# Optimization experiments

Measured on AMD Instinct MI355X. Metric: run time of the kernel, lower is better.

The kernel has to match this reference:

```python
import jax, jax.numpy as jnp
import numpy as np


def setup_inputs() -> dict:
    key = jax.random.key(0)
    kq, kk, kv = jax.random.split(key, 3)
    B, T, H, D = 2, 4096, 8, 64
    q = jax.random.normal(kq, (B, T, H, D), dtype=jnp.float32)
    k = jax.random.normal(kk, (B, T, H, D), dtype=jnp.float32)
    v = jax.random.normal(kv, (B, T, H, D), dtype=jnp.float32)
    return {"q": q, "k": k, "v": v}


def reference(q, k, v):
    """Linear matrix-memory recurrence over the sequence:
       M_t = M_{t-1} + v_t k_t^T ;  y_t = M_t q_t
    q, k, v: [B, T, H, D] -> y: [B, T, H, D]
    """
    B, T, H, D = q.shape
    # time-major for scan: [T, B, H, D]
    qT = jnp.moveaxis(q, 1, 0)
    kT = jnp.moveaxis(k, 1, 0)
    vT = jnp.moveaxis(v, 1, 0)

    def step(M, qkv):
        q_t, k_t, v_t = qkv  # each [B, H, D]
        # update: M += v_t k_t^T  (outer product, 'bhd,bhe->bhde')
        M = M + v_t[..., :, None] * k_t[..., None, :]
        # apply: y_t = M q_t  ('bhde,bhe->bhd')
        y_t = jnp.einsum('bhde,bhe->bhd', M, q_t)
        return M, y_t

    M0 = jnp.zeros((B, H, D, D), dtype=q.dtype)
    _, ys = jax.lax.scan(step, M0, (qT, kT, vT))  # ys: [T, B, H, D]
    return jnp.moveaxis(ys, 0, 1)  # [B, T, H, D]
```

## Files before the change

kernel.cpp:

```cpp
#include <hip/hip_runtime.h>


#define B_   2
#define T_   4096
#define H_   8
#define D_   64
#define CH   64
#define NC   (T_ / CH)
#define BH   (B_ * H_)
#define SROW (H_ * D_)
#define SB   (T_ * H_ * D_)

typedef __attribute__((ext_vector_type(4))) float f32x4;
typedef __attribute__((ext_vector_type(8))) short bf16x8;

__device__ inline unsigned short f2bf(float f) {
  unsigned int u = __builtin_bit_cast(unsigned int, f);
  unsigned int r = (u + 0x7FFFu + ((u >> 16) & 1u)) >> 16;
  return (unsigned short)r;
}
__device__ inline float bf2f(unsigned short b) {
  unsigned int u = ((unsigned int)b) << 16;
  return __builtin_bit_cast(float, u);
}
__device__ inline void st4bf(unsigned short* p, float a, float b, float c, float d) {
  union { uint2 u; unsigned short s[4]; } x;
  x.s[0] = f2bf(a); x.s[1] = f2bf(b); x.s[2] = f2bf(c); x.s[3] = f2bf(d);
  *(uint2*)p = x.u;
}
__device__ inline bf16x8 ld128(const unsigned short* p) {
  union { uint4 u; bf16x8 v; } x;
  x.u = *(const uint4*)p;
  return x.v;
}


__global__ __launch_bounds__(256) void k_chunksum(const float* __restrict__ kp,
                                                  const float* __restrict__ vp,
                                                  float* __restrict__ W) {
  const int bid = blockIdx.x;
  const int c   = bid % NC;
  const int bh  = bid / NC;
  const int b   = bh / H_, h = bh % H_;
  const size_t base = (size_t)b * SB + (size_t)h * D_ + (size_t)(c * CH) * SROW;

  __shared__ __align__(16) unsigned short KH[4096], KL[4096], VH[4096], VL[4096];

  const int tid = threadIdx.x;
  const int l = tid & 63, w = tid >> 6;
  const int mlan = l & 15, qlan = l >> 4;

  {
    const int t0 = (tid >> 4) * 4;
    const int m0 = tid & 15;
    const int qs = (t0 >> 3) & 3, kbs = t0 >> 5, j0 = t0 & 4;
    float4 kr[4], vr[4];
#pragma unroll
    for (int i = 0; i < 4; ++i) {
      const size_t g = base + (size_t)(t0 + i) * SROW + 4 * m0;
      kr[i] = *(const float4*)(kp + g);
      vr[i] = *(const float4*)(vp + g);
    }
#pragma unroll
    for (int r = 0; r < 4; ++r) {
      const int d = 4 * m0 + r;
      const int slot = r * 16 + qs * 4 + (m0 & 3);
      const int addr = (((d >> 4) * 2 + kbs) * 64 + slot) * 8 + j0;
      float ke[4] = { ((const float*)&kr[0])[r], ((const float*)&kr[1])[r],
                      ((const float*)&kr[2])[r], ((const float*)&kr[3])[r] };
      float ve[4] = { ((const float*)&vr[0])[r], ((const float*)&vr[1])[r],
                      ((const float*)&vr[2])[r], ((const float*)&vr[3])[r] };
      float kh[4], vh[4];
#pragma unroll
      for (int i = 0; i < 4; ++i) { kh[i] = bf2f(f2bf(ke[i])); vh[i] = bf2f(f2bf(ve[i])); }
      st4bf(KH + addr, kh[0], kh[1], kh[2], kh[3]);
      st4bf(KL + addr, ke[0] - kh[0], ke[1] - kh[1], ke[2] - kh[2], ke[3] - kh[3]);
      st4bf(VH + addr, vh[0], vh[1], vh[2], vh[3]);
      st4bf(VL + addr, ve[0] - vh[0], ve[1] - vh[1], ve[2] - vh[2], ve[3] - vh[3]);
    }
  }
  __syncthreads();

  const int rslot = ((mlan & 3) << 4) + (qlan << 2) + (mlan >> 2);

  bf16x8 avh[2], avl[2];
#pragma unroll
  for (int kb = 0; kb < 2; ++kb) {
    avh[kb] = ld128(VH + ((w * 2 + kb) * 64 + rslot) * 8);
    avl[kb] = ld128(VL + ((w * 2 + kb) * 64 + rslot) * 8);
  }
  float* Wc = W + (size_t)bid * (D_ * D_);
#pragma unroll
  for (int te = 0; te < 4; ++te) {
    f32x4 acc = {0.f, 0.f, 0.f, 0.f};
#pragma unroll
    for (int kb = 0; kb < 2; ++kb) {
      bf16x8 bkh = ld128(KH + ((te * 2 + kb) * 64 + rslot) * 8);
      bf16x8 bkl = ld128(KL + ((te * 2 + kb) * 64 + rslot) * 8);
      acc = __builtin_amdgcn_mfma_f32_16x16x32_bf16(avh[kb], bkh, acc, 0, 0, 0);
      acc = __builtin_amdgcn_mfma_f32_16x16x32_bf16(avl[kb], bkh, acc, 0, 0, 0);
      acc = __builtin_amdgcn_mfma_f32_16x16x32_bf16(avh[kb], bkl, acc, 0, 0, 0);
    }
#pragma unroll
    for (int r = 0; r < 4; ++r)
      Wc[(16 * w + 4 * qlan + r) * D_ + 16 * te + mlan] = acc[r];
  }
}

__global__ __launch_bounds__(256) void k_prefix(float* __restrict__ W) {
  const int g = blockIdx.x * 256 + threadIdx.x;
  float* base = W + (size_t)(g >> 12) * (NC * D_ * D_) + (g & 4095);
  float run = 0.f;
#pragma unroll
  for (int grp = 0; grp < 4; ++grp) {
    float v[16];
#pragma unroll
    for (int i = 0; i < 16; ++i)
      v[i] = base[(size_t)(grp * 16 + i) * (D_ * D_)];
#pragma unroll
    for (int i = 0; i < 16; ++i) {
      base[(size_t)(grp * 16 + i) * (D_ * D_)] = run;
      run += v[i];
    }
  }
}

__global__ __launch_bounds__(256) void k_output(const float* __restrict__ qp,
                                                const float* __restrict__ kp,
                                                const float* __restrict__ vp,
                                                const float* __restrict__ W,
                                                float* __restrict__ yp) {
  const int bid = blockIdx.x;
  const int c   = bid % NC;
  const int bh  = bid / NC;
  const int b   = bh / H_, h = bh % H_;
  const size_t base = (size_t)b * SB + (size_t)h * D_ + (size_t)(c * CH) * SROW;

  __shared__ __align__(16) unsigned short QF[4096], KF[4096], VF[4096],
                                          MH[4096], ML[4096], PS[64 * 72];

  const int tid = threadIdx.x;
  const int l = tid & 63, w = tid >> 6;
  const int mlan = l & 15, qlan = l >> 4;

#pragma unroll
  for (int it = 0; it < 4; ++it) {
    const int f = tid + it * 256;
    const int t = f >> 4, m0 = f & 15;
    const int kb = m0 >> 3, q = (m0 & 7) >> 1, j0 = (m0 & 1) * 4;
    const int addr = (((t >> 4) * 2 + kb) * 64 + ((t & 15) * 4 + q)) * 8 + j0;
    const size_t g = base + (size_t)t * SROW + 4 * m0;
    float4 qv = *(const float4*)(qp + g);
    float4 kv = *(const float4*)(kp + g);
    st4bf(QF + addr, qv.x, qv.y, qv.z, qv.w);
    st4bf(KF + addr, kv.x, kv.y, kv.z, kv.w);
    float4 mv = *(const float4*)(W + (size_t)bid * (D_ * D_) + t * D_ + 4 * m0);
    float mh[4] = { bf2f(f2bf(mv.x)), bf2f(f2bf(mv.y)), bf2f(f2bf(mv.z)), bf2f(f2bf(mv.w)) };
    st4bf(MH + addr, mh[0], mh[1], mh[2], mh[3]);
    st4bf(ML + addr, mv.x - mh[0], mv.y - mh[1], mv.z - mh[2], mv.w - mh[3]);
  }
  {
    const int s0 = (tid >> 4) * 4;
    const int m0 = tid & 15;
    const int qs = (s0 >> 3) & 3, kbs = s0 >> 5, j0 = s0 & 4;
    float4 vr[4];
#pragma unroll
    for (int i = 0; i < 4; ++i)
      vr[i] = *(const float4*)(vp + base + (size_t)(s0 + i) * SROW + 4 * m0);
#pragma unroll
    for (int r = 0; r < 4; ++r) {
      const int d = 4 * m0 + r;
      const int slot = r * 16 + qs * 4 + (m0 & 3);
      const int addr = (((d >> 4) * 2 + kbs) * 64 + slot) * 8 + j0;
      st4bf(VF + addr, ((const float*)&vr[0])[r], ((const float*)&vr[1])[r],
                       ((const float*)&vr[2])[r], ((const float*)&vr[3])[r]);
    }
  }
  __syncthreads();

  bf16x8 aq[2];
#pragma unroll
  for (int kb = 0; kb < 2; ++kb)
    aq[kb] = ld128(QF + ((w * 2 + kb) * 64 + (mlan * 4 + qlan)) * 8);

  f32x4 accP[4];
#pragma unroll
  for (int ts = 0; ts < 4; ++ts) accP[ts] = (f32x4){0.f, 0.f, 0.f, 0.f};
#pragma unroll
  for (int ts = 0; ts < 4; ++ts) {
    if (ts <= w) {
#pragma unroll
      for (int kb = 0; kb < 2; ++kb) {
        bf16x8 bk = ld128(KF + ((ts * 2 + kb) * 64 + (mlan * 4 + qlan)) * 8);
        accP[ts] = __builtin_amdgcn_mfma_f32_16x16x32_bf16(aq[kb], bk, accP[ts], 0, 0, 0);
      }
    }
  }
#pragma unroll
  for (int ts = 0; ts < 4; ++ts) {
    if (ts == w) {
#pragma unroll
      for (int r = 0; r < 4; ++r)
        if (mlan > qlan * 4 + r) accP[ts][r] = 0.f;
    }
  }
#pragma unroll
  for (int ts = 0; ts < 4; ++ts)
#pragma unroll
    for (int r = 0; r < 4; ++r)
      PS[(16 * w + 4 * qlan + r) * 72 + 16 * ts + mlan] = f2bf(accP[ts][r]);

  bf16x8 ap[2];
#pragma unroll
  for (int sb = 0; sb < 2; ++sb)
    ap[sb] = ld128(PS + (16 * w + mlan) * 72 + 32 * sb + 8 * qlan);

  const int rslot = ((mlan & 3) << 4) + (qlan << 2) + (mlan >> 2);

  f32x4 accY[4];
#pragma unroll
  for (int td = 0; td < 4; ++td) accY[td] = (f32x4){0.f, 0.f, 0.f, 0.f};

#pragma unroll
  for (int td = 0; td < 4; ++td)
#pragma unroll
    for (int sb = 0; sb < 2; ++sb) {
      bf16x8 bv = ld128(VF + ((td * 2 + sb) * 64 + rslot) * 8);
      accY[td] = __builtin_amdgcn_mfma_f32_16x16x32_bf16(ap[sb], bv, accY[td], 0, 0, 0);
    }
#pragma unroll
  for (int td = 0; td < 4; ++td)
#pragma unroll
    for (int kb = 0; kb < 2; ++kb) {
      bf16x8 bmh = ld128(MH + ((td * 2 + kb) * 64 + (mlan * 4 + qlan)) * 8);
      accY[td] = __builtin_amdgcn_mfma_f32_16x16x32_bf16(aq[kb], bmh, accY[td], 0, 0, 0);
      bf16x8 bml = ld128(ML + ((td * 2 + kb) * 64 + (mlan * 4 + qlan)) * 8);
      accY[td] = __builtin_amdgcn_mfma_f32_16x16x32_bf16(aq[kb], bml, accY[td], 0, 0, 0);
    }

#pragma unroll
  for (int td = 0; td < 4; ++td)
#pragma unroll
    for (int r = 0; r < 4; ++r)
      yp[base + (size_t)(16 * w + 4 * qlan + r) * SROW + 16 * td + mlan] = accY[td][r];
}

extern "C" void kernel_launch(void* const* d_in, const int* in_sizes, int n_in,
                              void* d_out, int out_size, void* d_ws, size_t ws_size,
                              hipStream_t stream) {
  const float* q = (const float*)d_in[0];
  const float* k = (const float*)d_in[1];
  const float* v = (const float*)d_in[2];
  float* y = (float*)d_out;
  float* W = (float*)d_ws;

  k_chunksum<<<BH * NC, 256, 0, stream>>>(k, v, W);
  k_prefix  <<<256, 256, 0, stream>>>(W);
  k_output  <<<BH * NC, 256, 0, stream>>>(q, k, v, W, y);
}
```

Before: 111.6 us.

## Store chunk sums in bf16 and prefix state as packed hi/lo bf16 pairs

The chunk-sum kernel now computes with a single bf16 MFMA per block instead of the three-term hi/lo split, and writes the chunk state as bf16 rather than fp32. The prefix kernel accumulates in fp32 and emits packed hi/lo bf16 pairs, which the output kernel loads straight into registers and unpacks, skipping the shared-memory staging of M. The P staging layout is also rearranged per wave. This cuts MFMA work, global traffic and LDS use, at the cost of lower precision in the per-chunk outer-product sums.

```diff
diff --git a/kernel.cpp b/kernel.cpp
--- a/kernel.cpp
+++ b/kernel.cpp
@@ -33,18 +33,29 @@
   x.u = *(const uint4*)p;
   return x.v;
 }
+__device__ inline void unpackM(const uint4 a, const uint4 b, bf16x8& hi, bf16x8& lo) {
+  unsigned xs[8] = { a.x, a.y, a.z, a.w, b.x, b.y, b.z, b.w };
+  union { unsigned u[4]; bf16x8 v; } H, L;
+#pragma unroll
+  for (int i = 0; i < 4; ++i) {
+    unsigned p0 = xs[2 * i], p1 = xs[2 * i + 1];
+    H.u[i] = (p0 >> 16) | (p1 & 0xffff0000u);
+    L.u[i] = (p0 & 0xffffu) | (p1 << 16);
+  }
+  hi = H.v; lo = L.v;
+}
 
 
 __global__ __launch_bounds__(256) void k_chunksum(const float* __restrict__ kp,
                                                   const float* __restrict__ vp,
-                                                  float* __restrict__ W) {
+                                                  unsigned short* __restrict__ Sp) {
   const int bid = blockIdx.x;
-  const int c   = bid % NC;
-  const int bh  = bid / NC;
-  const int b   = bh / H_, h = bh % H_;
+  const int c   = bid & 63;
+  const int bh  = bid >> 6;
+  const int b   = bh >> 3, h = bh & 7;
   const size_t base = (size_t)b * SB + (size_t)h * D_ + (size_t)(c * CH) * SROW;
 
-  __shared__ __align__(16) unsigned short KH[4096], KL[4096], VH[4096], VL[4096];
+  __shared__ __align__(16) unsigned short KT[4096], VT[4096];
 
   const int tid = threadIdx.x;
   const int l = tid & 63, w = tid >> 6;
@@ -66,61 +77,53 @@
       const int d = 4 * m0 + r;
       const int slot = r * 16 + qs * 4 + (m0 & 3);
       const int addr = (((d >> 4) * 2 + kbs) * 64 + slot) * 8 + j0;
-      float ke[4] = { ((const float*)&kr[0])[r], ((const float*)&kr[1])[r],
-                      ((const float*)&kr[2])[r], ((const float*)&kr[3])[r] };
-      float ve[4] = { ((const float*)&vr[0])[r], ((const float*)&vr[1])[r],
-                      ((const float*)&vr[2])[r], ((const float*)&vr[3])[r] };
-      float kh[4], vh[4];
-#pragma unroll
-      for (int i = 0; i < 4; ++i) { kh[i] = bf2f(f2bf(ke[i])); vh[i] = bf2f(f2bf(ve[i])); }
-      st4bf(KH + addr, kh[0], kh[1], kh[2], kh[3]);
-      st4bf(KL + addr, ke[0] - kh[0], ke[1] - kh[1], ke[2] - kh[2], ke[3] - kh[3]);
-      st4bf(VH + addr, vh[0], vh[1], vh[2], vh[3]);
-      st4bf(VL + addr, ve[0] - vh[0], ve[1] - vh[1], ve[2] - vh[2], ve[3] - vh[3]);
+      st4bf(KT + addr, ((const float*)&kr[0])[r], ((const float*)&kr[1])[r],
+                       ((const float*)&kr[2])[r], ((const float*)&kr[3])[r]);
+      st4bf(VT + addr, ((const float*)&vr[0])[r], ((const float*)&vr[1])[r],
+                       ((const float*)&vr[2])[r], ((const float*)&vr[3])[r]);
     }
   }
   __syncthreads();
 
   const int rslot = ((mlan & 3) << 4) + (qlan << 2) + (mlan >> 2);
-
-  bf16x8 avh[2], avl[2];
-#pragma unroll
-  for (int kb = 0; kb < 2; ++kb) {
-    avh[kb] = ld128(VH + ((w * 2 + kb) * 64 + rslot) * 8);
-    avl[kb] = ld128(VL + ((w * 2 + kb) * 64 + rslot) * 8);
-  }
-  float* Wc = W + (size_t)bid * (D_ * D_);
+  bf16x8 av[2];
+  av[0] = ld128(VT + ((w * 2 + 0) * 64 + rslot) * 8);
+  av[1] = ld128(VT + ((w * 2 + 1) * 64 + rslot) * 8);
+
+  unsigned short* Sc = Sp + (size_t)bid * 4096;
 #pragma unroll
   for (int te = 0; te < 4; ++te) {
     f32x4 acc = {0.f, 0.f, 0.f, 0.f};
 #pragma unroll
     for (int kb = 0; kb < 2; ++kb) {
-      bf16x8 bkh = ld128(KH + ((te * 2 + kb) * 64 + rslot) * 8);
-      bf16x8 bkl = ld128(KL + ((te * 2 + kb) * 64 + rslot) * 8);
-      acc = __builtin_amdgcn_mfma_f32_16x16x32_bf16(avh[kb], bkh, acc, 0, 0, 0);
-      acc = __builtin_amdgcn_mfma_f32_16x16x32_bf16(avl[kb], bkh, acc, 0, 0, 0);
-      acc = __builtin_amdgcn_mfma_f32_16x16x32_bf16(avh[kb], bkl, acc, 0, 0, 0);
+      bf16x8 bk = ld128(KT + ((te * 2 + kb) * 64 + rslot) * 8);
+      acc = __builtin_amdgcn_mfma_f32_16x16x32_bf16(av[kb], bk, acc, 0, 0, 0);
     }
 #pragma unroll
     for (int r = 0; r < 4; ++r)
-      Wc[(16 * w + 4 * qlan + r) * D_ + 16 * te + mlan] = acc[r];
-  }
-}
-
-__global__ __launch_bounds__(256) void k_prefix(float* __restrict__ W) {
+      Sc[(16 * w + 4 * qlan + r) * 64 + 16 * te + mlan] = f2bf(acc[r]);
+  }
+}
+
+__global__ __launch_bounds__(256) void k_prefix(const unsigned short* __restrict__ Sp,
+                                                unsigned* __restrict__ Mp) {
   const int g = blockIdx.x * 256 + threadIdx.x;
-  float* base = W + (size_t)(g >> 12) * (NC * D_ * D_) + (g & 4095);
+  const int bh = g >> 12, e = g & 4095;
+  const unsigned short* sp = Sp + (size_t)bh * (NC * 4096) + e;
+  unsigned* mp = Mp + (size_t)bh * (NC * 4096) + e;
   float run = 0.f;
 #pragma unroll
   for (int grp = 0; grp < 4; ++grp) {
-    float v[16];
+    unsigned short sv[16];
 #pragma unroll
     for (int i = 0; i < 16; ++i)
-      v[i] = base[(size_t)(grp * 16 + i) * (D_ * D_)];
+      sv[i] = sp[(size_t)(grp * 16 + i) * 4096];
 #pragma unroll
     for (int i = 0; i < 16; ++i) {
-      base[(size_t)(grp * 16 + i) * (D_ * D_)] = run;
-      run += v[i];
+      const unsigned short hi = f2bf(run);
+      const unsigned short lo = f2bf(run - bf2f(hi));
+      mp[(size_t)(grp * 16 + i) * 4096] = ((unsigned)hi << 16) | (unsigned)lo;
+      run += bf2f(sv[i]);
     }
   }
 }
@@ -128,36 +131,42 @@
 __global__ __launch_bounds__(256) void k_output(const float* __restrict__ qp,
                                                 const float* __restrict__ kp,
                                                 const float* __restrict__ vp,
-                                                const float* __restrict__ W,
+                                                const unsigned* __restrict__ Mp,
                                                 float* __restrict__ yp) {
   const int bid = blockIdx.x;
-  const int c   = bid % NC;
-  const int bh  = bid / NC;
-  const int b   = bh / H_, h = bh % H_;
+  const int c   = bid & 63;
+  const int bh  = bid >> 6;
+  const int b   = bh >> 3, h = bh & 7;
   const size_t base = (size_t)b * SB + (size_t)h * D_ + (size_t)(c * CH) * SROW;
 
-  __shared__ __align__(16) unsigned short QF[4096], KF[4096], VF[4096],
-                                          MH[4096], ML[4096], PS[64 * 72];
+  __shared__ __align__(16) unsigned short QF[4096], KF[4096], VF[4096], PS[4096];
 
   const int tid = threadIdx.x;
   const int l = tid & 63, w = tid >> 6;
   const int mlan = l & 15, qlan = l >> 4;
 
+  uint4 mA[8], mB[8];
+#pragma unroll
+  for (int td = 0; td < 4; ++td)
+#pragma unroll
+    for (int kb = 0; kb < 2; ++kb) {
+      const uint4* mp = (const uint4*)(Mp + (size_t)bid * 4096
+                                      + (16 * td + mlan) * 64 + 32 * kb + 8 * qlan);
+      mA[td * 2 + kb] = mp[0];
+      mB[td * 2 + kb] = mp[1];
+    }
+
 #pragma unroll
   for (int it = 0; it < 4; ++it) {
     const int f = tid + it * 256;
     const int t = f >> 4, m0 = f & 15;
-    const int kb = m0 >> 3, q = (m0 & 7) >> 1, j0 = (m0 & 1) * 4;
-    const int addr = (((t >> 4) * 2 + kb) * 64 + ((t & 15) * 4 + q)) * 8 + j0;
+    const int kb = m0 >> 3, qq = (m0 & 7) >> 1, j0 = (m0 & 1) * 4;
+    const int addr = (((t >> 4) * 2 + kb) * 64 + ((t & 15) * 4 + qq)) * 8 + j0;
     const size_t g = base + (size_t)t * SROW + 4 * m0;
     float4 qv = *(const float4*)(qp + g);
     float4 kv = *(const float4*)(kp + g);
     st4bf(QF + addr, qv.x, qv.y, qv.z, qv.w);
     st4bf(KF + addr, kv.x, kv.y, kv.z, kv.w);
-    float4 mv = *(const float4*)(W + (size_t)bid * (D_ * D_) + t * D_ + 4 * m0);
-    float mh[4] = { bf2f(f2bf(mv.x)), bf2f(f2bf(mv.y)), bf2f(f2bf(mv.z)), bf2f(f2bf(mv.w)) };
-    st4bf(MH + addr, mh[0], mh[1], mh[2], mh[3]);
-    st4bf(ML + addr, mv.x - mh[0], mv.y - mh[1], mv.z - mh[2], mv.w - mh[3]);
   }
   {
     const int s0 = (tid >> 4) * 4;
@@ -197,23 +206,26 @@
     }
   }
 #pragma unroll
-  for (int ts = 0; ts < 4; ++ts) {
+  for (int ts = 0; ts < 4; ++ts)
     if (ts == w) {
 #pragma unroll
       for (int r = 0; r < 4; ++r)
         if (mlan > qlan * 4 + r) accP[ts][r] = 0.f;
     }
-  }
-#pragma unroll
-  for (int ts = 0; ts < 4; ++ts)
-#pragma unroll
-    for (int r = 0; r < 4; ++r)
-      PS[(16 * w + 4 * qlan + r) * 72 + 16 * ts + mlan] = f2bf(accP[ts][r]);
-
+
+  {
+    unsigned short* PSW = PS + w * 1024;
+#pragma unroll
+    for (int ts = 0; ts < 4; ++ts)
+#pragma unroll
+      for (int r = 0; r < 4; ++r)
+        PSW[((2 * ts + (mlan >> 3)) * 16 + 4 * qlan + r) * 8 + (mlan & 7)] =
+            f2bf(accP[ts][r]);
+  }
   bf16x8 ap[2];
 #pragma unroll
   for (int sb = 0; sb < 2; ++sb)
-    ap[sb] = ld128(PS + (16 * w + mlan) * 72 + 32 * sb + 8 * qlan);
+    ap[sb] = ld128(PS + w * 1024 + ((4 * sb + qlan) * 16 + mlan) * 8);
 
   const int rslot = ((mlan & 3) << 4) + (qlan << 2) + (mlan >> 2);
 
@@ -232,9 +244,9 @@
   for (int td = 0; td < 4; ++td)
 #pragma unroll
     for (int kb = 0; kb < 2; ++kb) {
-      bf16x8 bmh = ld128(MH + ((td * 2 + kb) * 64 + (mlan * 4 + qlan)) * 8);
+      bf16x8 bmh, bml;
+      unpackM(mA[td * 2 + kb], mB[td * 2 + kb], bmh, bml);
       accY[td] = __builtin_amdgcn_mfma_f32_16x16x32_bf16(aq[kb], bmh, accY[td], 0, 0, 0);
-      bf16x8 bml = ld128(ML + ((td * 2 + kb) * 64 + (mlan * 4 + qlan)) * 8);
       accY[td] = __builtin_amdgcn_mfma_f32_16x16x32_bf16(aq[kb], bml, accY[td], 0, 0, 0);
     }
 
@@ -252,9 +264,10 @@
   const float* k = (const float*)d_in[1];
   const float* v = (const float*)d_in[2];
   float* y = (float*)d_out;
-  float* W = (float*)d_ws;
-
-  k_chunksum<<<BH * NC, 256, 0, stream>>>(k, v, W);
-  k_prefix  <<<256, 256, 0, stream>>>(W);
-  k_output  <<<BH * NC, 256, 0, stream>>>(q, k, v, W, y);
-}
+  unsigned short* S = (unsigned short*)d_ws;
+  unsigned*       M = (unsigned*)((char*)d_ws + (32u << 20));
+
+  k_chunksum<<<BH * NC, 256, 0, stream>>>(k, v, S);
+  k_prefix  <<<256, 256, 0, stream>>>(S, M);
+  k_output  <<<BH * NC, 256, 0, stream>>>(q, k, v, M, y);
+}
```

New measurement: 110.8 us. No clear change (-0.7%).
